# Optimization experiments

Measured on AMD Instinct MI355X. Metric: run time of the kernel, lower is better.

Reference implementation:

```python
import jax, jax.numpy as jnp
import numpy as np
from jax import lax

K = 7            # pool_size / PSROI_BINS
C_OUT = 10       # output channels per bin (features has K*K*C_OUT channels)
FEAT_STRIDE = 16
LAMDA = 0.1
SAMPLES = 2      # bilinear sample points per bin side
H = W = 200
C_IN = K * K * C_OUT  # 490
N_ROIS = 512


def setup_inputs() -> dict:
    key = jax.random.key(0)
    k1, k2, k3, k4 = jax.random.split(key, 4)
    features = jax.random.normal(k1, (1, H, W, C_IN), jnp.float32)
    conv_w = jax.random.truncated_normal(k2, -2.0, 2.0, (3, 3, C_IN, 2 * K * K), jnp.float32) * 0.01
    img = H * FEAT_STRIDE  # image-space extent
    cxy = jax.random.uniform(k3, (N_ROIS, 2), minval=0.0, maxval=img - 1.0)
    wh = jax.random.uniform(k4, (N_ROIS, 2), minval=64.0, maxval=640.0)
    x1 = jnp.clip(cxy[:, 0] - wh[:, 0] * 0.5, 0.0, img - 2.0)
    y1 = jnp.clip(cxy[:, 1] - wh[:, 1] * 0.5, 0.0, img - 2.0)
    x2 = jnp.clip(x1 + wh[:, 0], x1 + 1.0, img - 1.0)
    y2 = jnp.clip(y1 + wh[:, 1], y1 + 1.0, img - 1.0)
    rois = jnp.stack([jnp.zeros(N_ROIS), x1, y1, x2, y2], axis=-1)  # [N,5]
    return {"features": features, "rois": rois, "conv_w": conv_w}


def _bilinear(feat, y, x):
    """feat [H,W,C]; y,x arbitrary equal shapes -> [..., C]."""
    Hf, Wf = feat.shape[0], feat.shape[1]
    y = jnp.clip(y, 0.0, Hf - 1.0)
    x = jnp.clip(x, 0.0, Wf - 1.0)
    y0 = jnp.floor(y)
    x0 = jnp.floor(x)
    y0i = y0.astype(jnp.int32)
    x0i = x0.astype(jnp.int32)
    y1i = jnp.minimum(y0i + 1, Hf - 1)
    x1i = jnp.minimum(x0i + 1, Wf - 1)
    wy = (y - y0)[..., None]
    wx = (x - x0)[..., None]
    v00 = feat[y0i, x0i]
    v01 = feat[y0i, x1i]
    v10 = feat[y1i, x0i]
    v11 = feat[y1i, x1i]
    return (v00 * (1 - wy) * (1 - wx) + v01 * (1 - wy) * wx
            + v10 * wy * (1 - wx) + v11 * wy * wx)


def _ps_roi(feat, box, cpg, offsets):
    """Position-sensitive RoI avg pooling with optional per-bin offsets.
    feat [H,W,K*K*cpg]; box (x1,y1,x2,y2) image coords; offsets [K,K,2] (dx,dy)
    in image coords or None. Returns [K,K,cpg]."""
    x1, y1, x2, y2 = box
    fx1 = x1 / FEAT_STRIDE
    fy1 = y1 / FEAT_STRIDE
    bw = (x2 - x1 + 1.0) / FEAT_STRIDE / K
    bh = (y2 - y1 + 1.0) / FEAT_STRIDE / K
    idx = jnp.arange(K, dtype=feat.dtype)
    s = (jnp.arange(SAMPLES, dtype=feat.dtype) + 0.5) / SAMPLES
    sx = fx1 + (idx[:, None] + s[None, :]) * bw  # [K(j), S]
    sy = fy1 + (idx[:, None] + s[None, :]) * bh  # [K(i), S]
    gx = jnp.broadcast_to(sx[None, :, None, :], (K, K, SAMPLES, SAMPLES))
    gy = jnp.broadcast_to(sy[:, None, :, None], (K, K, SAMPLES, SAMPLES))
    if offsets is not None:
        off = offsets / FEAT_STRIDE  # image -> feature coords
        gx = gx + off[..., 0][:, :, None, None]
        gy = gy + off[..., 1][:, :, None, None]
    vals = _bilinear(feat, gy, gx)                     # [K,K,S,S,K*K*cpg]
    vals = vals.reshape(K, K, SAMPLES, SAMPLES, K * K, cpg)
    bin_idx = (jnp.arange(K)[:, None] * K + jnp.arange(K)[None, :])  # [K,K]
    sel = jnp.take_along_axis(
        vals, bin_idx[:, :, None, None, None, None], axis=4)[..., 0, :]
    return sel.mean(axis=(2, 3))  # [K,K,cpg]


def reference(features, rois, conv_w):
    # 3x3 same conv producing 2*K*K offset channels (no bias)
    offset_map = lax.conv_general_dilated(
        features, conv_w, (1, 1), 'SAME',
        dimension_numbers=('NHWC', 'HWIO', 'NHWC'))[0]  # [H,W,2*K*K]
    feat0 = features[0]  # [H,W,K*K*C_OUT]

    def one_roi(roi):
        x1, y1, x2, y2 = roi[1], roi[2], roi[3], roi[4]
        rw = x2 - x1 + 1.0
        rh = y2 - y1 + 1.0
        box = (x1, y1, x2, y2)
        # stage 1: pool the offset map position-sensitively -> [K,K,2]
        off = _ps_roi(offset_map, box, 2, None).reshape(-1, 2)
        off = jnp.stack((off[:, 0] * rw * LAMDA,
                         off[:, 1] * rh * LAMDA), axis=-1).reshape(K, K, 2)
        # stage 2: deformable PS-RoI pooling of the features -> [K,K,C_OUT]
        return _ps_roi(feat0, box, C_OUT, off)

    return jax.vmap(one_roi)(rois)  # [N, K, K, C_OUT]
```

## Files before the change

kernel.cpp:

```cpp
#include <hip/hip_runtime.h>
#include <hip/hip_bf16.h>

#define Hh   200
#define Ww   200
#define CIN  490
#define OCN  98
#define KK   7
#define COUT 10
#define NROIS 512
#define PIX  8

#define PH   202
#define PW   202
#define PC   512
#define NPIX (Hh * Ww)
#define KCN  16
#define NF   7
#define NUNITS 144
#define HGRAN  18
#define HALF_SHORTS (8 * 3584)

typedef __attribute__((ext_vector_type(8))) short short8;
typedef __attribute__((ext_vector_type(4))) float float4v;

__global__ __launch_bounds__(256) void pack_feat_kernel(
    const float* __restrict__ feat, __hip_bfloat16* __restrict__ pf)
{
    int tid = blockIdx.x * 256 + threadIdx.x;
    if (tid >= PH * PW * (PC / 8)) return;
    int c8  = (tid & 63) * 8;
    int pix = tid >> 6;
    int py = pix / PW, px = pix % PW;
    __hip_bfloat16* dst = pf + (size_t)pix * PC + c8;
    bool interior = (py >= 1 && py <= Hh && px >= 1 && px <= Ww);

    __hip_bfloat16 v[8];
    if (interior && c8 + 8 <= CIN) {
        const float* s = feat + ((size_t)(py - 1) * Ww + (px - 1)) * CIN + c8;
#pragma unroll
        for (int q = 0; q < 4; ++q) {
            float2 f2 = *reinterpret_cast<const float2*>(s + q * 2);
            v[q * 2]     = __float2bfloat16(f2.x);
            v[q * 2 + 1] = __float2bfloat16(f2.y);
        }
    } else {
        const float* s = interior ? feat + ((size_t)(py - 1) * Ww + (px - 1)) * CIN : nullptr;
#pragma unroll
        for (int j = 0; j < 8; ++j) {
            float val = (interior && (c8 + j) < CIN) ? s[c8 + j] : 0.f;
            v[j] = __float2bfloat16(val);
        }
    }
    *reinterpret_cast<short8*>(dst) = *reinterpret_cast<short8*>(v);
}

__global__ __launch_bounds__(256) void pack_w_kernel(
    const float* __restrict__ w, __hip_bfloat16* __restrict__ bp)
{
    int idx = blockIdx.x * 256 + threadIdx.x;
    if (idx >= NUNITS * NF * 64 * 8) return;
    int j = idx & 7;
    int l = (idx >> 3) & 63;
    int f = (idx >> 9) % NF;
    int u = idx / (NF * 512);
    int kc = u / 9, tap = u % 9;
    int k = kc * 32 + ((l >> 4) * 8) + j;
    int n = f * 16 + (l & 15);
    float val = (k < CIN && n < OCN) ? w[((size_t)tap * CIN + k) * OCN + n] : 0.f;
    bp[idx] = __float2bfloat16(val);
}

__global__ __launch_bounds__(640, 2) void conv_mfma_kernel(
    const short* __restrict__ pf,
    const short* __restrict__ bp,
    float* __restrict__ om)
{
    __shared__ short bsm[2 * HALF_SHORTS];

    int orig = blockIdx.x;
    int xcd = orig & 7;
    int pos = orig >> 3;
    int blk = ((xcd < 2) ? xcd * 32 : 64 + (xcd - 2) * 31) + pos;

    int l = threadIdx.x & 63;
    int w = threadIdx.x >> 6;
    int mpos = w % 5;
    int ks = w / 5;
    int ubase = ks * 72;
    int m0 = blk * 160 + mpos * 32;

    const short* abase0;
    const short* abase1;
    {
        int row0 = m0 + (l & 15);
        int row1 = m0 + 16 + (l & 15);
        int y0 = row0 / Ww, x0 = row0 % Ww;
        int y1 = row1 / Ww, x1 = row1 % Ww;
        abase0 = pf + ((size_t)(y0 * PW + x0) * PC) + ((l >> 4) * 8);
        abase1 = pf + ((size_t)(y1 * PW + x1) * PC) + ((l >> 4) * 8);
    }

    float4v acc[2][NF];
#pragma unroll
    for (int r = 0; r < 2; ++r)
#pragma unroll
        for (int f = 0; f < NF; ++f) acc[r][f] = (float4v){0.f, 0.f, 0.f, 0.f};

    auto aOff = [&](int u) -> int {
        int kc = u / 9, tap = u - kc * 9;
        int ky = tap / 3, kx = tap - ky * 3;
        return (ky * PW + kx) * PC + kc * 32;
    };
    int lbase = ks * HALF_SHORTS;

#pragma unroll
    for (int s = 0; s < 6; ++s) {
        int i = mpos + s * 5;
        if (i < 28) {
            int uu = ubase + i / 7, f = i % 7;
            short8 v = *reinterpret_cast<const short8*>(
                bp + ((size_t)(uu * NF + f)) * 512 + l * 8);
            *reinterpret_cast<short8*>(
                &bsm[lbase + (uu & 7) * 3584 + f * 512 + l * 8]) = v;
        }
    }
    short8 a00 = *reinterpret_cast<const short8*>(abase0 + aOff(ubase + 0));
    short8 a01 = *reinterpret_cast<const short8*>(abase0 + aOff(ubase + 1));
    short8 a02 = *reinterpret_cast<const short8*>(abase0 + aOff(ubase + 2));
    short8 a03 = *reinterpret_cast<const short8*>(abase0 + aOff(ubase + 3));
    short8 a10 = *reinterpret_cast<const short8*>(abase1 + aOff(ubase + 0));
    short8 a11 = *reinterpret_cast<const short8*>(abase1 + aOff(ubase + 1));
    short8 a12 = *reinterpret_cast<const short8*>(abase1 + aOff(ubase + 2));
    short8 a13 = *reinterpret_cast<const short8*>(abase1 + aOff(ubase + 3));
    __syncthreads();

    for (int g = 0; g < HGRAN; ++g) {
        bool more = (g < HGRAN - 1);
        int u0n = ubase + (g + 1) * 4;

        short8 st0, st1, st2, st3, st4, st5;
        int off0 = -1, off1 = -1, off2 = -1, off3 = -1, off4 = -1, off5 = -1;
        if (more) {
#define STAGE_LOAD(S, STV, OFFV)                                               \
            {                                                                  \
                int i = mpos + (S) * 5;                                        \
                if (i < 28) {                                                  \
                    int uu = u0n + i / 7, f = i % 7;                           \
                    STV = *reinterpret_cast<const short8*>(                    \
                        bp + ((size_t)(uu * NF + f)) * 512 + l * 8);           \
                    OFFV = lbase + (uu & 7) * 3584 + f * 512 + l * 8;          \
                }                                                              \
            }
            STAGE_LOAD(0, st0, off0)
            STAGE_LOAD(1, st1, off1)
            STAGE_LOAD(2, st2, off2)
            STAGE_LOAD(3, st3, off3)
            STAGE_LOAD(4, st4, off4)
            STAGE_LOAD(5, st5, off5)
#undef STAGE_LOAD
        }

        int u0 = ubase + g * 4;
#define UNIT_STEP(J, AR0, AR1)                                                  \
        {                                                                       \
            int sbase = lbase + ((u0 + J) & 7) * 3584 + l * 8;                  \
            _Pragma("unroll")                                                   \
            for (int f = 0; f < NF; ++f) {                                      \
                short8 b = *reinterpret_cast<short8*>(&bsm[sbase + f * 512]);   \
                acc[0][f] = __builtin_amdgcn_mfma_f32_16x16x32_bf16(            \
                    AR0, b, acc[0][f], 0, 0, 0);                                \
                acc[1][f] = __builtin_amdgcn_mfma_f32_16x16x32_bf16(            \
                    AR1, b, acc[1][f], 0, 0, 0);                                \
            }                                                                   \
            if (more) {                                                         \
                AR0 = *reinterpret_cast<const short8*>(abase0 + aOff(u0n + J)); \
                AR1 = *reinterpret_cast<const short8*>(abase1 + aOff(u0n + J)); \
            }                                                                   \
        }
        UNIT_STEP(0, a00, a10)
        UNIT_STEP(1, a01, a11)
        UNIT_STEP(2, a02, a12)
        UNIT_STEP(3, a03, a13)
#undef UNIT_STEP

        if (off0 >= 0) *reinterpret_cast<short8*>(&bsm[off0]) = st0;
        if (off1 >= 0) *reinterpret_cast<short8*>(&bsm[off1]) = st1;
        if (off2 >= 0) *reinterpret_cast<short8*>(&bsm[off2]) = st2;
        if (off3 >= 0) *reinterpret_cast<short8*>(&bsm[off3]) = st3;
        if (off4 >= 0) *reinterpret_cast<short8*>(&bsm[off4]) = st4;
        if (off5 >= 0) *reinterpret_cast<short8*>(&bsm[off5]) = st5;
        __syncthreads();
    }

    float* lred = (float*)bsm;
    if (ks == 1) {
#pragma unroll
        for (int r = 0; r < 2; ++r)
#pragma unroll
            for (int f = 0; f < NF; ++f) {
                int idx = (((mpos * 2 + r) * NF + f) * 64 + l) * 4;
                *reinterpret_cast<float4v*>(&lred[idx]) = acc[r][f];
            }
    }
    __syncthreads();
    if (ks == 0) {
        int n = l & 15;
#pragma unroll
        for (int r = 0; r < 2; ++r) {
            int rbase = m0 + r * 16 + ((l >> 4) * 4);
#pragma unroll
            for (int f = 0; f < NF; ++f) {
                int idx = (((mpos * 2 + r) * NF + f) * 64 + l) * 4;
                float4v other = *reinterpret_cast<float4v*>(&lred[idx]);
                float4v tot = acc[r][f] + other;
                int col = f * 16 + n;
                if (col < OCN) {
#pragma unroll
                    for (int j = 0; j < 4; ++j)
                        om[(size_t)(rbase + j) * OCN + col] = tot[j];
                }
            }
        }
    }
}

__global__ __launch_bounds__(256) void conv3x3_kernel(
    const float* __restrict__ feat, const float* __restrict__ w,
    const float* __restrict__ zero, float* __restrict__ om)
{
    int idx = blockIdx.x * blockDim.x + threadIdx.x;
    if (idx >= Hh * (Ww / PIX) * OCN) return;
    int oc = idx % OCN;
    int g  = idx / OCN;
    int x0 = (g % (Ww / PIX)) * PIX;
    int y  = g / (Ww / PIX);

    float acc[PIX];
#pragma unroll
    for (int p = 0; p < PIX; ++p) acc[p] = 0.f;

    for (int ky = 0; ky < 3; ++ky) {
        int yy = y + ky - 1;
        if (yy < 0 || yy >= Hh) continue;
        const float* frow = feat + (size_t)yy * Ww * CIN;
        for (int kx = 0; kx < 3; ++kx) {
            const float* wp = w + ((ky * 3 + kx) * CIN) * OCN + oc;
            const float* fp[PIX];
#pragma unroll
            for (int p = 0; p < PIX; ++p) {
                int xx = x0 + p + kx - 1;
                fp[p] = (xx >= 0 && xx < Ww) ? (frow + (size_t)xx * CIN) : zero;
            }
            for (int ic = 0; ic < CIN; ic += 2) {
                float w0 = wp[ic * OCN];
                float w1 = wp[(ic + 1) * OCN];
#pragma unroll
                for (int p = 0; p < PIX; ++p) {
                    float2 f = *reinterpret_cast<const float2*>(fp[p] + ic);
                    acc[p] = fmaf(f.x, w0, acc[p]);
                    acc[p] = fmaf(f.y, w1, acc[p]);
                }
            }
        }
    }
    float* orow = om + ((size_t)y * Ww + x0) * OCN + oc;
#pragma unroll
    for (int p = 0; p < PIX; ++p) orow[p * OCN] = acc[p];
}

__device__ __forceinline__ void bilin_setup(float y, float x,
    int& i00, int& i01, int& i10, int& i11,
    float& w00, float& w01, float& w10, float& w11)
{
    y = fminf(fmaxf(y, 0.f), 199.f);
    x = fminf(fmaxf(x, 0.f), 199.f);
    float y0f = floorf(y), x0f = floorf(x);
    int y0 = (int)y0f, x0i = (int)x0f;
    int y1 = min(y0 + 1, 199), x1 = min(x0i + 1, 199);
    float wy = y - y0f, wx = x - x0f;
    i00 = y0 * Ww + x0i;  i01 = y0 * Ww + x1;
    i10 = y1 * Ww + x0i;  i11 = y1 * Ww + x1;
    w00 = (1.f - wy) * (1.f - wx);
    w01 = (1.f - wy) * wx;
    w10 = wy * (1.f - wx);
    w11 = wy * wx;
}

__global__ __launch_bounds__(256) void psroi_kernel(
    const float* __restrict__ feat, const float* __restrict__ rois,
    const float* __restrict__ om, float* __restrict__ out)
{
    int n = blockIdx.x;
    int t = threadIdx.x;

    float x1 = rois[n * 5 + 1], y1 = rois[n * 5 + 2];
    float x2 = rois[n * 5 + 3], y2 = rois[n * 5 + 4];
    float rw = x2 - x1 + 1.0f, rh = y2 - y1 + 1.0f;
    float fx1 = x1 * 0.0625f, fy1 = y1 * 0.0625f;
    float bw = (rw * 0.0625f) / 7.0f;
    float bh = (rh * 0.0625f) / 7.0f;

    __shared__ float offs[49][2];

    if (t < 49) {
        int bi = t / 7, bj = t % 7;
        float ax = 0.f, ay = 0.f;
#pragma unroll
        for (int ss = 0; ss < 4; ++ss) {
            float sj = ((float)(ss & 1) + 0.5f) * 0.5f;
            float si = ((float)(ss >> 1) + 0.5f) * 0.5f;
            float gx = fx1 + ((float)bj + sj) * bw;
            float gy = fy1 + ((float)bi + si) * bh;
            int i00, i01, i10, i11; float w00, w01, w10, w11;
            bilin_setup(gy, gx, i00, i01, i10, i11, w00, w01, w10, w11);
            int c0 = t * 2;
            const float* p00 = om + (size_t)i00 * OCN + c0;
            const float* p01 = om + (size_t)i01 * OCN + c0;
            const float* p10 = om + (size_t)i10 * OCN + c0;
            const float* p11 = om + (size_t)i11 * OCN + c0;
            ax += w00 * p00[0] + w01 * p01[0] + w10 * p10[0] + w11 * p11[0];
            ay += w00 * p00[1] + w01 * p01[1] + w10 * p10[1] + w11 * p11[1];
        }
        offs[t][0] = ax * 0.25f * rw * 0.1f * 0.0625f;
        offs[t][1] = ay * 0.25f * rh * 0.1f * 0.0625f;
    }
    __syncthreads();

    for (int o = t; o < KK * KK * COUT; o += blockDim.x) {
        int bin = o / COUT, c = o % COUT;
        int bi = bin / 7, bj = bin % 7;
        float dx = offs[bin][0], dy = offs[bin][1];
        int ch = bin * COUT + c;
        float acc = 0.f;
#pragma unroll
        for (int ss = 0; ss < 4; ++ss) {
            float sj = ((float)(ss & 1) + 0.5f) * 0.5f;
            float si = ((float)(ss >> 1) + 0.5f) * 0.5f;
            float gx = fx1 + ((float)bj + sj) * bw + dx;
            float gy = fy1 + ((float)bi + si) * bh + dy;
            int i00, i01, i10, i11; float w00, w01, w10, w11;
            bilin_setup(gy, gx, i00, i01, i10, i11, w00, w01, w10, w11);
            acc += w00 * feat[(size_t)i00 * CIN + ch]
                 + w01 * feat[(size_t)i01 * CIN + ch]
                 + w10 * feat[(size_t)i10 * CIN + ch]
                 + w11 * feat[(size_t)i11 * CIN + ch];
        }
        out[(size_t)n * (KK * KK * COUT) + o] = acc * 0.25f;
    }
}

extern "C" void kernel_launch(void* const* d_in, const int* in_sizes, int n_in,
                              void* d_out, int out_size, void* d_ws, size_t ws_size,
                              hipStream_t stream) {
    const float* feat = (const float*)d_in[0];
    const float* rois = (const float*)d_in[1];
    const float* w    = (const float*)d_in[2];
    float* out = (float*)d_out;

    const size_t OM_BYTES = (size_t)NPIX * OCN * 4;
    const size_t BP_BYTES = (size_t)NUNITS * NF * 64 * 8 * 2;
    const size_t PF_BYTES = (size_t)PH * PW * PC * 2;
    const size_t NEEDED = OM_BYTES + BP_BYTES + PF_BYTES;

    if (ws_size >= NEEDED) {
        float* om = (float*)d_ws;
        __hip_bfloat16* bp = (__hip_bfloat16*)((char*)d_ws + OM_BYTES);
        __hip_bfloat16* pf = (__hip_bfloat16*)((char*)d_ws + OM_BYTES + BP_BYTES);

        int wThreads = NUNITS * NF * 64 * 8;
        pack_w_kernel<<<(wThreads + 255) / 256, 256, 0, stream>>>(w, bp);
        int fThreads = PH * PW * (PC / 8);
        pack_feat_kernel<<<(fThreads + 255) / 256, 256, 0, stream>>>(feat, pf);
        conv_mfma_kernel<<<250, 640, 0, stream>>>(
            (const short*)pf, (const short*)bp, om);
        psroi_kernel<<<NROIS, 256, 0, stream>>>(feat, rois, om, out);
    } else {
        float* zero = (float*)d_ws;
        float* om   = (float*)d_ws + 1024;
        hipMemsetAsync(d_ws, 0, 4096, stream);
        int convThreads = Hh * (Ww / PIX) * OCN;
        conv3x3_kernel<<<(convThreads + 255) / 256, 256, 0, stream>>>(feat, w, zero, om);
        psroi_kernel<<<NROIS, 256, 0, stream>>>(feat, rois, om, out);
    }
}
```

Before: 97.21 us.

## Merge pack kernels, prefetch conv A-fragments early, vectorize PSROI channel pairs

New measurement: 101.5 us. +4.5%, slower.

```diff
diff --git a/kernel.cpp b/kernel.cpp
--- a/kernel.cpp
+++ b/kernel.cpp
@@ -20,54 +20,54 @@
 #define HGRAN  18
 #define HALF_SHORTS (8 * 3584)
 
+#define FEAT_BLOCKS 10201
+#define W_BLOCKS    2016
+
 typedef __attribute__((ext_vector_type(8))) short short8;
 typedef __attribute__((ext_vector_type(4))) float float4v;
 
-__global__ __launch_bounds__(256) void pack_feat_kernel(
-    const float* __restrict__ feat, __hip_bfloat16* __restrict__ pf)
-{
-    int tid = blockIdx.x * 256 + threadIdx.x;
-    if (tid >= PH * PW * (PC / 8)) return;
-    int c8  = (tid & 63) * 8;
-    int pix = tid >> 6;
-    int py = pix / PW, px = pix % PW;
-    __hip_bfloat16* dst = pf + (size_t)pix * PC + c8;
-    bool interior = (py >= 1 && py <= Hh && px >= 1 && px <= Ww);
-
-    __hip_bfloat16 v[8];
-    if (interior && c8 + 8 <= CIN) {
-        const float* s = feat + ((size_t)(py - 1) * Ww + (px - 1)) * CIN + c8;
-#pragma unroll
-        for (int q = 0; q < 4; ++q) {
-            float2 f2 = *reinterpret_cast<const float2*>(s + q * 2);
-            v[q * 2]     = __float2bfloat16(f2.x);
-            v[q * 2 + 1] = __float2bfloat16(f2.y);
-        }
+__global__ __launch_bounds__(256) void pack_all_kernel(
+    const float* __restrict__ feat, const float* __restrict__ w,
+    __hip_bfloat16* __restrict__ pf, __hip_bfloat16* __restrict__ bp)
+{
+    if (blockIdx.x < FEAT_BLOCKS) {
+        int tid = blockIdx.x * 256 + threadIdx.x;
+        int c8  = (tid & 63) * 8;
+        int pix = tid >> 6;
+        int py = pix / PW, px = pix % PW;
+        __hip_bfloat16* dst = pf + (size_t)pix * PC + c8;
+        bool interior = (py >= 1 && py <= Hh && px >= 1 && px <= Ww);
+
+        __hip_bfloat16 v[8];
+        if (interior && c8 + 8 <= CIN) {
+            const float* s = feat + ((size_t)(py - 1) * Ww + (px - 1)) * CIN + c8;
+#pragma unroll
+            for (int q = 0; q < 4; ++q) {
+                float2 f2 = *reinterpret_cast<const float2*>(s + q * 2);
+                v[q * 2]     = __float2bfloat16(f2.x);
+                v[q * 2 + 1] = __float2bfloat16(f2.y);
+            }
+        } else {
+            const float* s = interior ? feat + ((size_t)(py - 1) * Ww + (px - 1)) * CIN : nullptr;
+#pragma unroll
+            for (int j = 0; j < 8; ++j) {
+                float val = (interior && (c8 + j) < CIN) ? s[c8 + j] : 0.f;
+                v[j] = __float2bfloat16(val);
+            }
+        }
+        *reinterpret_cast<short8*>(dst) = *reinterpret_cast<short8*>(v);
     } else {
-        const float* s = interior ? feat + ((size_t)(py - 1) * Ww + (px - 1)) * CIN : nullptr;
-#pragma unroll
-        for (int j = 0; j < 8; ++j) {
-            float val = (interior && (c8 + j) < CIN) ? s[c8 + j] : 0.f;
-            v[j] = __float2bfloat16(val);
-        }
-    }
-    *reinterpret_cast<short8*>(dst) = *reinterpret_cast<short8*>(v);
-}
-
-__global__ __launch_bounds__(256) void pack_w_kernel(
-    const float* __restrict__ w, __hip_bfloat16* __restrict__ bp)
-{
-    int idx = blockIdx.x * 256 + threadIdx.x;
-    if (idx >= NUNITS * NF * 64 * 8) return;
-    int j = idx & 7;
-    int l = (idx >> 3) & 63;
-    int f = (idx >> 9) % NF;
-    int u = idx / (NF * 512);
-    int kc = u / 9, tap = u % 9;
-    int k = kc * 32 + ((l >> 4) * 8) + j;
-    int n = f * 16 + (l & 15);
-    float val = (k < CIN && n < OCN) ? w[((size_t)tap * CIN + k) * OCN + n] : 0.f;
-    bp[idx] = __float2bfloat16(val);
+        int idx = (blockIdx.x - FEAT_BLOCKS) * 256 + threadIdx.x;
+        int j = idx & 7;
+        int l = (idx >> 3) & 63;
+        int f = (idx >> 9) % NF;
+        int u = idx / (NF * 512);
+        int kc = u / 9, tap = u % 9;
+        int k = kc * 32 + ((l >> 4) * 8) + j;
+        int n = f * 16 + (l & 15);
+        float val = (k < CIN && n < OCN) ? w[((size_t)tap * CIN + k) * OCN + n] : 0.f;
+        bp[idx] = __float2bfloat16(val);
+    }
 }
 
 __global__ __launch_bounds__(640, 2) void conv_mfma_kernel(
@@ -159,6 +159,17 @@
             STAGE_LOAD(5, st5, off5)
 #undef STAGE_LOAD
         }
+        short8 n00, n01, n02, n03, n10, n11, n12, n13;
+        if (more) {
+            n00 = *reinterpret_cast<const short8*>(abase0 + aOff(u0n + 0));
+            n01 = *reinterpret_cast<const short8*>(abase0 + aOff(u0n + 1));
+            n02 = *reinterpret_cast<const short8*>(abase0 + aOff(u0n + 2));
+            n03 = *reinterpret_cast<const short8*>(abase0 + aOff(u0n + 3));
+            n10 = *reinterpret_cast<const short8*>(abase1 + aOff(u0n + 0));
+            n11 = *reinterpret_cast<const short8*>(abase1 + aOff(u0n + 1));
+            n12 = *reinterpret_cast<const short8*>(abase1 + aOff(u0n + 2));
+            n13 = *reinterpret_cast<const short8*>(abase1 + aOff(u0n + 3));
+        }
 
         int u0 = ubase + g * 4;
 #define UNIT_STEP(J, AR0, AR1)                                                  \
@@ -172,10 +183,6 @@
                 acc[1][f] = __builtin_amdgcn_mfma_f32_16x16x32_bf16(            \
                     AR1, b, acc[1][f], 0, 0, 0);                                \
             }                                                                   \
-            if (more) {                                                         \
-                AR0 = *reinterpret_cast<const short8*>(abase0 + aOff(u0n + J)); \
-                AR1 = *reinterpret_cast<const short8*>(abase1 + aOff(u0n + J)); \
-            }                                                                   \
         }
         UNIT_STEP(0, a00, a10)
         UNIT_STEP(1, a01, a11)
@@ -189,6 +196,10 @@
         if (off3 >= 0) *reinterpret_cast<short8*>(&bsm[off3]) = st3;
         if (off4 >= 0) *reinterpret_cast<short8*>(&bsm[off4]) = st4;
         if (off5 >= 0) *reinterpret_cast<short8*>(&bsm[off5]) = st5;
+        if (more) {
+            a00 = n00; a01 = n01; a02 = n02; a03 = n03;
+            a10 = n10; a11 = n11; a12 = n12; a13 = n13;
+        }
         __syncthreads();
     }
 
@@ -326,12 +337,12 @@
     }
     __syncthreads();
 
-    for (int o = t; o < KK * KK * COUT; o += blockDim.x) {
-        int bin = o / COUT, c = o % COUT;
+    if (t < 245) {
+        int bin = t / 5, cp = t % 5;
         int bi = bin / 7, bj = bin % 7;
         float dx = offs[bin][0], dy = offs[bin][1];
-        int ch = bin * COUT + c;
-        float acc = 0.f;
+        int ch0 = bin * COUT + cp * 2;
+        float accx = 0.f, accy = 0.f;
 #pragma unroll
         for (int ss = 0; ss < 4; ++ss) {
             float sj = ((float)(ss & 1) + 0.5f) * 0.5f;
@@ -340,12 +351,16 @@
             float gy = fy1 + ((float)bi + si) * bh + dy;
             int i00, i01, i10, i11; float w00, w01, w10, w11;
             bilin_setup(gy, gx, i00, i01, i10, i11, w00, w01, w10, w11);
-            acc += w00 * feat[(size_t)i00 * CIN + ch]
-                 + w01 * feat[(size_t)i01 * CIN + ch]
-                 + w10 * feat[(size_t)i10 * CIN + ch]
-                 + w11 * feat[(size_t)i11 * CIN + ch];
-        }
-        out[(size_t)n * (KK * KK * COUT) + o] = acc * 0.25f;
+            float2 v00 = *reinterpret_cast<const float2*>(feat + (size_t)i00 * CIN + ch0);
+            float2 v01 = *reinterpret_cast<const float2*>(feat + (size_t)i01 * CIN + ch0);
+            float2 v10 = *reinterpret_cast<const float2*>(feat + (size_t)i10 * CIN + ch0);
+            float2 v11 = *reinterpret_cast<const float2*>(feat + (size_t)i11 * CIN + ch0);
+            accx += w00 * v00.x + w01 * v01.x + w10 * v10.x + w11 * v11.x;
+            accy += w00 * v00.y + w01 * v01.y + w10 * v10.y + w11 * v11.y;
+        }
+        float2 res = {accx * 0.25f, accy * 0.25f};
+        *reinterpret_cast<float2*>(
+            out + (size_t)n * (KK * KK * COUT) + bin * COUT + cp * 2) = res;
     }
 }
 
@@ -367,10 +382,7 @@
         __hip_bfloat16* bp = (__hip_bfloat16*)((char*)d_ws + OM_BYTES);
         __hip_bfloat16* pf = (__hip_bfloat16*)((char*)d_ws + OM_BYTES + BP_BYTES);
 
-        int wThreads = NUNITS * NF * 64 * 8;
-        pack_w_kernel<<<(wThreads + 255) / 256, 256, 0, stream>>>(w, bp);
-        int fThreads = PH * PW * (PC / 8);
-        pack_feat_kernel<<<(fThreads + 255) / 256, 256, 0, stream>>>(feat, pf);
+        pack_all_kernel<<<FEAT_BLOCKS + W_BLOCKS, 256, 0, stream>>>(feat, w, pf, bp);
         conv_mfma_kernel<<<250, 640, 0, stream>>>(
             (const short*)pf, (const short*)bp, om);
         psroi_kernel<<<NROIS, 256, 0, stream>>>(feat, rois, om, out);
```
